# Optimization experiments

Measured on AMD Instinct MI355X. Metric: run time of the kernel, lower is better.

The kernel has to match this reference:

```python
import jax, jax.numpy as jnp
import numpy as np

E, D, DFF = 8, 1024, 4096

def setup_inputs() -> dict:
    key = jax.random.key(0)
    ks = jax.random.split(key, 10)
    s = 0.02
    return {
        "x":  jax.random.normal(ks[0], (4, 2048, D), dtype=jnp.float32),
        "Wr": jax.random.normal(ks[1], (D, E), dtype=jnp.float32) * s,
        "br": jnp.zeros((E,), dtype=jnp.float32),
        "W1": jax.random.normal(ks[2], (E, D, DFF), dtype=jnp.float32) * s,
        "b1": jnp.zeros((E, DFF), dtype=jnp.float32),
        "W2": jax.random.normal(ks[3], (E, D, DFF), dtype=jnp.float32) * s,
        "b2": jnp.zeros((E, DFF), dtype=jnp.float32),
        "W3": jax.random.normal(ks[4], (E, DFF, D), dtype=jnp.float32) * s,
        "b3": jnp.zeros((E, D), dtype=jnp.float32),
    }

def reference(x, Wr, br, W1, b1, W2, b2, W3, b3):
    b, s, d = x.shape
    xt = x.reshape(b * s, d)                       # [T, D]
    logits = xt @ Wr + br                          # [T, E]
    pr, idx = jax.lax.top_k(logits, 2)             # [T, 2]
    w = jax.nn.softmax(pr, axis=-1)                # softmax over the 2 selected experts
    # combine weight per (token, expert): sum of routing weights where expert selected
    onehot = jax.nn.one_hot(idx, W1.shape[0], dtype=x.dtype)  # [T, 2, E]
    cw = jnp.einsum('tk,tke->te', w, onehot)       # [T, E]
    y = jnp.zeros_like(xt)
    for e in range(W1.shape[0]):                   # small fixed expert loop
        h = jax.nn.silu(xt @ W1[e] + b1[e]) * (xt @ W2[e] + b2[e])  # SwiGLU [T, DFF]
        y = y + (h @ W3[e] + b3[e]) * cw[:, e:e + 1]
    return y.reshape(b, s, d)
```

## Files before the change

kernel.cpp:

```cpp
#include <hip/hip_runtime.h>

#define T_TOK 8192
#define DIM   1024
#define DFF_  4096
#define NE    8
#define MAXT  144

typedef float  f32x4 __attribute__((ext_vector_type(4)));
typedef __bf16 b16x8 __attribute__((ext_vector_type(8)));
typedef unsigned short u16x4 __attribute__((ext_vector_type(4)));

__device__ __forceinline__ unsigned short f2bf(float f) {
  union { float f; unsigned int u; } v; v.f = f;
  unsigned int r = v.u + 0x7fffu + ((v.u >> 16) & 1u);
  return (unsigned short)(r >> 16);
}

__device__ __forceinline__ void gload_lds16(const void* g, void* l) {
  __builtin_amdgcn_global_load_lds((const __attribute__((address_space(1))) void*)g,
                                   (__attribute__((address_space(3))) void*)l,
                                   16, 0, 0);
}

#define DRAIN_VMCNT() asm volatile("s_waitcnt vmcnt(0)" ::: "memory")

__global__ __launch_bounds__(256) void transpose_cvt(const float* __restrict__ src,
                                                     unsigned short* __restrict__ dst,
                                                     int R, int C) {
  __shared__ float tile[64][68];
  size_t mat = (size_t)blockIdx.z * R * C;
  int c0 = blockIdx.x * 64, r0 = blockIdx.y * 64;
  int t = threadIdx.x;
  int rcol = (t & 15) * 4, rrow = t >> 4;
  const float* s = src + mat + (size_t)r0 * C + c0;
#pragma unroll
  for (int i = 0; i < 4; i++) {
    int r = rrow + i * 16;
    f32x4 v = *(const f32x4*)(s + (size_t)r * C + rcol);
    *(f32x4*)(&tile[r][rcol]) = v;
  }
  __syncthreads();
  unsigned short* d = dst + mat + (size_t)c0 * R + r0;
  int wrow4 = (t & 15) * 4, wcol = t >> 4;
#pragma unroll
  for (int i = 0; i < 4; i++) {
    int cc = wcol + i * 16;
    u16x4 o;
    o[0] = f2bf(tile[wrow4 + 0][cc]);
    o[1] = f2bf(tile[wrow4 + 1][cc]);
    o[2] = f2bf(tile[wrow4 + 2][cc]);
    o[3] = f2bf(tile[wrow4 + 3][cc]);
    *(u16x4*)(&d[(size_t)cc * R + wrow4]) = o;
  }
}

__global__ __launch_bounds__(256) void router_k(const float* __restrict__ x,
                                                const float* __restrict__ Wr,
                                                const float* __restrict__ br,
                                                unsigned short* __restrict__ Xbf,
                                                int* __restrict__ top2e,
                                                float* __restrict__ top2w,
                                                int* __restrict__ counts) {
  __shared__ int lcnt[NE];
  if (threadIdx.x < NE) lcnt[threadIdx.x] = 0;
  __syncthreads();
  int wid = threadIdx.x >> 6, lane = threadIdx.x & 63;
  int t = blockIdx.x * 4 + wid;
  const float* xr = x + (size_t)t * DIM;
  unsigned short* xb = Xbf + (size_t)t * DIM;
  float s[NE];
#pragma unroll
  for (int e = 0; e < NE; e++) s[e] = 0.f;
  for (int i = 0; i < DIM / 64; i++) {
    int dd = i * 64 + lane;
    float xv = xr[dd];
    xb[dd] = f2bf(xv);
    const float* w = Wr + (size_t)dd * NE;
#pragma unroll
    for (int e = 0; e < NE; e++) s[e] += xv * w[e];
  }
#pragma unroll
  for (int m = 32; m >= 1; m >>= 1) {
#pragma unroll
    for (int e = 0; e < NE; e++) s[e] += __shfl_xor(s[e], m, 64);
  }
  if (lane == 0) {
#pragma unroll
    for (int e = 0; e < NE; e++) s[e] += br[e];
    int e0 = 0;
#pragma unroll
    for (int e = 1; e < NE; e++) if (s[e] > s[e0]) e0 = e;
    int e1 = (e0 == 0) ? 1 : 0;
#pragma unroll
    for (int e = 0; e < NE; e++) if (e != e0 && s[e] > s[e1]) e1 = e;
    float w0 = 1.f / (1.f + expf(s[e1] - s[e0]));
    top2e[2 * t] = e0; top2e[2 * t + 1] = e1;
    top2w[2 * t] = w0; top2w[2 * t + 1] = 1.f - w0;
    atomicAdd(&lcnt[e0], 1);
    atomicAdd(&lcnt[e1], 1);
  }
  __syncthreads();
  if (threadIdx.x < NE) atomicAdd(&counts[threadIdx.x], lcnt[threadIdx.x]);
}

__global__ void scan_build(int* __restrict__ ctrl) {
  if (threadIdx.x != 0 || blockIdx.x != 0) return;
  int* counts = ctrl;
  int* offsets = ctrl + 8;
  int* cursors = ctrl + 16;
  int* nt256 = ctrl + 24;
  int* tE256 = ctrl + 32;
  int* tM256 = ctrl + 32 + MAXT;
  int o = 0;
  for (int e = 0; e < NE; e++) { offsets[e] = o; cursors[e] = o; o += counts[e]; }
  int a = 0;
  for (int e = 0; e < NE; e++)
    for (int m0 = 0; m0 < counts[e]; m0 += 256) { tE256[a] = e; tM256[a] = m0; a++; }
  nt256[0] = a;
}

__global__ __launch_bounds__(256) void scatter_k(const int* __restrict__ top2e,
                                                 const float* __restrict__ top2w,
                                                 int* __restrict__ cursors,
                                                 int* __restrict__ list_tok,
                                                 float* __restrict__ list_w) {
  __shared__ int lcnt[NE];
  __shared__ int lbase[NE];
  int tid = threadIdx.x;
  if (tid < NE) lcnt[tid] = 0;
  __syncthreads();
  int t = blockIdx.x * 256 + tid;
  int e0 = top2e[2 * t], e1 = top2e[2 * t + 1];
  int r0 = atomicAdd(&lcnt[e0], 1);
  int r1 = atomicAdd(&lcnt[e1], 1);
  __syncthreads();
  if (tid < NE) lbase[tid] = atomicAdd(&cursors[tid], lcnt[tid]);
  __syncthreads();
  int p0 = lbase[e0] + r0, p1 = lbase[e1] + r1;
  list_tok[p0] = t; list_w[p0] = top2w[2 * t];
  list_tok[p1] = t; list_w[p1] = top2w[2 * t + 1];
}

__global__ __launch_bounds__(1024, 4) void gemm1_k(const unsigned short* __restrict__ Xbf,
                                                   const unsigned short* __restrict__ W1T,
                                                   const unsigned short* __restrict__ W2T,
                                                   const float* __restrict__ b1,
                                                   const float* __restrict__ b2,
                                                   unsigned short* __restrict__ H,
                                                   const int* __restrict__ list_tok,
                                                   const int* __restrict__ ctrl) {
  const int* counts = ctrl; const int* offsets = ctrl + 8;
  const int* ntile = ctrl + 24;
  const int* tileE = ctrl + 32; const int* tileM = ctrl + 32 + MAXT;
  int bt = blockIdx.y;
  if (bt >= ntile[0]) return;
  int e = tileE[bt], m0 = tileM[bt];
  int Me = counts[e], off = offsets[e];
  int n0 = blockIdx.x * 128;

  __shared__ unsigned short lds[2][32768];

  int tid = threadIdx.x, lane = tid & 63, wid = tid >> 6;
  int wr = wid >> 2, wc = wid & 3;

  const unsigned short* gsrc[4];
  unsigned ldsoff[4];
  {
    int lr = lane >> 3;
    int sc = ((lane & 7) ^ (lane >> 3)) * 8;
#pragma unroll
    for (int j = 0; j < 4; j++) {
      int c = wid * 4 + j;
      ldsoff[j] = c * 512;
      if (c < 32) {
        int r = c * 8 + lr;
        int tok = (m0 + r < Me) ? list_tok[off + m0 + r] : list_tok[off];
        gsrc[j] = Xbf + (size_t)tok * DIM + sc;
      } else if (c < 48) {
        int n = n0 + (c - 32) * 8 + lr;
        gsrc[j] = W1T + ((size_t)e * DFF_ + n) * DIM + sc;
      } else {
        int n = n0 + (c - 48) * 8 + lr;
        gsrc[j] = W2T + ((size_t)e * DFF_ + n) * DIM + sc;
      }
    }
  }

  unsigned aoff[2][4], boff[2][2];
  {
    int colg = lane >> 4;
#pragma unroll
    for (int kk = 0; kk < 2; kk++) {
#pragma unroll
      for (int m = 0; m < 4; m++) {
        int row = wr * 64 + m * 16 + (lane & 15);
        aoff[kk][m] = row * 64 + (((kk * 4 + colg) ^ (row & 7)) * 8);
      }
#pragma unroll
      for (int n = 0; n < 2; n++) {
        int row = wc * 32 + n * 16 + (lane & 15);
        boff[kk][n] = 16384 + row * 64 + (((kk * 4 + colg) ^ (row & 7)) * 8);
      }
    }
  }

  f32x4 acc1[4][2], acc2[4][2];
#pragma unroll
  for (int i = 0; i < 4; i++)
#pragma unroll
    for (int j = 0; j < 2; j++) {
      acc1[i][j] = f32x4{0.f, 0.f, 0.f, 0.f};
      acc2[i][j] = f32x4{0.f, 0.f, 0.f, 0.f};
    }

  auto compute = [&](const unsigned short* base) {
#pragma unroll
    for (int kk = 0; kk < 2; kk++) {
      b16x8 aF[4], bF1[2], bF2[2];
#pragma unroll
      for (int m = 0; m < 4; m++) aF[m] = *(const b16x8*)(base + aoff[kk][m]);
#pragma unroll
      for (int n = 0; n < 2; n++) {
        bF1[n] = *(const b16x8*)(base + boff[kk][n]);
        bF2[n] = *(const b16x8*)(base + boff[kk][n] + 8192);
      }
#pragma unroll
      for (int m = 0; m < 4; m++)
#pragma unroll
        for (int n = 0; n < 2; n++) {
          acc1[m][n] = __builtin_amdgcn_mfma_f32_16x16x32_bf16(aF[m], bF1[n], acc1[m][n], 0, 0, 0);
          acc2[m][n] = __builtin_amdgcn_mfma_f32_16x16x32_bf16(aF[m], bF2[n], acc2[m][n], 0, 0, 0);
        }
    }
  };

#pragma unroll
  for (int j = 0; j < 4; j++) gload_lds16(gsrc[j], (void*)(&lds[0][ldsoff[j]]));
  DRAIN_VMCNT();
  __syncthreads();

  int cur = 0;
  const int NK = DIM / 64;
  for (int kt = 0; kt < NK; kt++) {
    if (kt + 1 < NK) {
#pragma unroll
      for (int j = 0; j < 4; j++)
        gload_lds16(gsrc[j] + (kt + 1) * 64, (void*)(&lds[cur ^ 1][ldsoff[j]]));
    }
    compute(&lds[cur][0]);
    DRAIN_VMCNT();
    __syncthreads();
    cur ^= 1;
  }

#pragma unroll
  for (int n = 0; n < 2; n++) {
    int col = n0 + wc * 32 + n * 16 + (lane & 15);
    float bb1 = b1[e * DFF_ + col], bb2 = b2[e * DFF_ + col];
#pragma unroll
    for (int m = 0; m < 4; m++) {
      int rbase = wr * 64 + m * 16 + (lane >> 4) * 4;
#pragma unroll
      for (int r = 0; r < 4; r++) {
        int rr = rbase + r;
        if (m0 + rr < Me) {
          float c1 = acc1[m][n][r] + bb1;
          float c2 = acc2[m][n][r] + bb2;
          float h = c1 * c2 / (1.f + __expf(-c1));
          H[(size_t)(off + m0 + rr) * DFF_ + col] = f2bf(h);
        }
      }
    }
  }
}

__global__ __launch_bounds__(1024, 4) void gemm2_k(const unsigned short* __restrict__ H,
                                                   const unsigned short* __restrict__ W3T,
                                                   const float* __restrict__ b3,
                                                   const int* __restrict__ list_tok,
                                                   const float* __restrict__ list_w,
                                                   float* __restrict__ y,
                                                   const int* __restrict__ ctrl) {
  const int* counts = ctrl; const int* offsets = ctrl + 8;
  const int* ntile = ctrl + 24;
  const int* tileE = ctrl + 32; const int* tileM = ctrl + 32 + MAXT;
  int bt = blockIdx.y;
  if (bt >= ntile[0]) return;
  int e = tileE[bt], m0 = tileM[bt];
  int Me = counts[e], off = offsets[e];
  int n0 = blockIdx.x * 256;

  __shared__ unsigned short lds[2][32768];

  int tid = threadIdx.x, lane = tid & 63, wid = tid >> 6;
  int wr = wid >> 2, wc = wid & 3;

  const unsigned short* gsrc[4];
  unsigned ldsoff[4];
  {
    int lr = lane >> 3;
    int sc = ((lane & 7) ^ (lane >> 3)) * 8;
#pragma unroll
    for (int j = 0; j < 4; j++) {
      int c = wid * 4 + j;
      ldsoff[j] = c * 512;
      if (c < 32) {
        int r = c * 8 + lr;
        int pos = (m0 + r < Me) ? (off + m0 + r) : off;
        gsrc[j] = H + (size_t)pos * DFF_ + sc;
      } else {
        int n = n0 + (c - 32) * 8 + lr;
        gsrc[j] = W3T + ((size_t)e * DIM + n) * DFF_ + sc;
      }
    }
  }

  unsigned aoff[2][4], boff[2][4];
  {
    int colg = lane >> 4;
#pragma unroll
    for (int kk = 0; kk < 2; kk++) {
#pragma unroll
      for (int m = 0; m < 4; m++) {
        int row = wr * 64 + m * 16 + (lane & 15);
        aoff[kk][m] = row * 64 + (((kk * 4 + colg) ^ (row & 7)) * 8);
      }
#pragma unroll
      for (int n = 0; n < 4; n++) {
        int row = wc * 64 + n * 16 + (lane & 15);
        boff[kk][n] = 16384 + row * 64 + (((kk * 4 + colg) ^ (row & 7)) * 8);
      }
    }
  }

  f32x4 acc[4][4];
#pragma unroll
  for (int i = 0; i < 4; i++)
#pragma unroll
    for (int j = 0; j < 4; j++) acc[i][j] = f32x4{0.f, 0.f, 0.f, 0.f};

  auto compute = [&](const unsigned short* base) {
#pragma unroll
    for (int kk = 0; kk < 2; kk++) {
      b16x8 aF[4], bF[4];
#pragma unroll
      for (int m = 0; m < 4; m++) aF[m] = *(const b16x8*)(base + aoff[kk][m]);
#pragma unroll
      for (int n = 0; n < 4; n++) bF[n] = *(const b16x8*)(base + boff[kk][n]);
#pragma unroll
      for (int m = 0; m < 4; m++)
#pragma unroll
        for (int n = 0; n < 4; n++)
          acc[m][n] = __builtin_amdgcn_mfma_f32_16x16x32_bf16(aF[m], bF[n], acc[m][n], 0, 0, 0);
    }
  };

#pragma unroll
  for (int j = 0; j < 4; j++) gload_lds16(gsrc[j], (void*)(&lds[0][ldsoff[j]]));
  DRAIN_VMCNT();
  __syncthreads();

  int cur = 0;
  const int NK = DFF_ / 64;
  for (int kt = 0; kt < NK; kt++) {
    if (kt + 1 < NK) {
#pragma unroll
      for (int j = 0; j < 4; j++)
        gload_lds16(gsrc[j] + (kt + 1) * 64, (void*)(&lds[cur ^ 1][ldsoff[j]]));
    }
    compute(&lds[cur][0]);
    DRAIN_VMCNT();
    __syncthreads();
    cur ^= 1;
  }

#pragma unroll
  for (int n = 0; n < 4; n++) {
    int col = n0 + wc * 64 + n * 16 + (lane & 15);
    float bb3 = b3[e * DIM + col];
#pragma unroll
    for (int m = 0; m < 4; m++) {
      int rbase = wr * 64 + m * 16 + (lane >> 4) * 4;
#pragma unroll
      for (int r = 0; r < 4; r++) {
        int rr = rbase + r;
        if (m0 + rr < Me) {
          int pos = off + m0 + rr;
          float v = list_w[pos] * (acc[m][n][r] + bb3);
          atomicAdd(&y[(size_t)list_tok[pos] * DIM + col], v);
        }
      }
    }
  }
}

extern "C" void kernel_launch(void* const* d_in, const int* in_sizes, int n_in,
                              void* d_out, int out_size, void* d_ws, size_t ws_size,
                              hipStream_t stream) {
  (void)in_sizes; (void)n_in; (void)ws_size;
  const float* x  = (const float*)d_in[0];
  const float* Wr = (const float*)d_in[1];
  const float* br = (const float*)d_in[2];
  const float* W1 = (const float*)d_in[3];
  const float* b1 = (const float*)d_in[4];
  const float* W2 = (const float*)d_in[5];
  const float* b2 = (const float*)d_in[6];
  const float* W3 = (const float*)d_in[7];
  const float* b3 = (const float*)d_in[8];
  float* y = (float*)d_out;
  char* ws = (char*)d_ws;

  const size_t matB = (size_t)NE * DFF_ * DIM * 2;
  size_t oW1T = 0;
  size_t oW2T = oW1T + matB;
  size_t oXbf = oW2T + matB;
  size_t oH   = oXbf + (size_t)T_TOK * DIM * 2;
  size_t oT2e = oH + (size_t)2 * T_TOK * DFF_ * 2;
  size_t oT2w = oT2e + (size_t)2 * T_TOK * 4;
  size_t oLtk = oT2w + (size_t)2 * T_TOK * 4;
  size_t oLw  = oLtk + (size_t)2 * T_TOK * 4;
  size_t oCtl = oLw + (size_t)2 * T_TOK * 4;

  unsigned short* W1T = (unsigned short*)(ws + oW1T);
  unsigned short* W2T = (unsigned short*)(ws + oW2T);
  unsigned short* W3T = (unsigned short*)(ws + oW1T);
  unsigned short* Xbf = (unsigned short*)(ws + oXbf);
  unsigned short* Hb  = (unsigned short*)(ws + oH);
  int*   top2e = (int*)(ws + oT2e);
  float* top2w = (float*)(ws + oT2w);
  int*   ltok  = (int*)(ws + oLtk);
  float* lw    = (float*)(ws + oLw);
  int*   ctrl  = (int*)(ws + oCtl);

  hipMemsetAsync(y, 0, (size_t)out_size * 4, stream);
  hipMemsetAsync(ctrl, 0, (32 + 2 * MAXT) * 4, stream);

  transpose_cvt<<<dim3(DFF_ / 64, DIM / 64, NE), 256, 0, stream>>>(W1, W1T, DIM, DFF_);
  transpose_cvt<<<dim3(DFF_ / 64, DIM / 64, NE), 256, 0, stream>>>(W2, W2T, DIM, DFF_);
  router_k<<<dim3(T_TOK / 4), 256, 0, stream>>>(x, Wr, br, Xbf, top2e, top2w, ctrl);
  scan_build<<<dim3(1), 64, 0, stream>>>(ctrl);
  scatter_k<<<dim3(T_TOK / 256), 256, 0, stream>>>(top2e, top2w, ctrl + 16, ltok, lw);
  gemm1_k<<<dim3(DFF_ / 128, 71), 1024, 0, stream>>>(Xbf, W1T, W2T, b1, b2, Hb, ltok, ctrl);
  transpose_cvt<<<dim3(DIM / 64, DFF_ / 64, NE), 256, 0, stream>>>(W3, W3T, DFF_, DIM);
  gemm2_k<<<dim3(DIM / 256, 71), 1024, 0, stream>>>(Hb, W3T, b3, ltok, lw, y, ctrl);
}
```

Before: 706.7 us.

## Split-K gemm2, merge W1/W2 transposes, widen transpose and router accesses

gemm2 now splits the DFF reduction into two halves along grid z and accumulates both into y with atomics. Only the first half adds the bias, and the grid grows from 284 to 568 blocks to fill more CUs. The W1 and W2 transpose-convert launches are merged into one kernel. The transpose now uses an XOR-swizzled LDS tile with 8-wide bf16 stores, and the router loads x as float4 and writes four bf16 values at once. The cost is twice as many atomicAdds into y, and the order of float accumulation now varies between runs.

```diff
diff --git a/kernel.cpp b/kernel.cpp
--- a/kernel.cpp
+++ b/kernel.cpp
@@ -9,6 +9,7 @@
 typedef float  f32x4 __attribute__((ext_vector_type(4)));
 typedef __bf16 b16x8 __attribute__((ext_vector_type(8)));
 typedef unsigned short u16x4 __attribute__((ext_vector_type(4)));
+typedef unsigned short u16x8 __attribute__((ext_vector_type(8)));
 
 __device__ __forceinline__ unsigned short f2bf(float f) {
   union { float f; unsigned int u; } v; v.f = f;
@@ -24,34 +25,54 @@
 
 #define DRAIN_VMCNT() asm volatile("s_waitcnt vmcnt(0)" ::: "memory")
 
+__device__ __forceinline__ void tcvt_body(const float* __restrict__ src,
+                                          unsigned short* __restrict__ dst,
+                                          int R, int C, int bx, int by) {
+  __shared__ float tile[64 * 64];
+  int c0 = bx * 64, r0 = by * 64;
+  int t = threadIdx.x;
+  const float* s = src + (size_t)r0 * C + c0;
+  int rrow = t >> 4, c4r = t & 15;
+#pragma unroll
+  for (int i = 0; i < 4; i++) {
+    int r = rrow + i * 16;
+    f32x4 v = *(const f32x4*)(s + (size_t)r * C + c4r * 4);
+    int c4s = c4r ^ (r >> 3);
+    *(f32x4*)(&tile[r * 64 + c4s * 4]) = v;
+  }
+  __syncthreads();
+  unsigned short* d = dst + (size_t)c0 * R + r0;
+  int wr8 = (t & 7) * 8, wcol = t >> 3;
+#pragma unroll
+  for (int i = 0; i < 2; i++) {
+    int cc = wcol + i * 32;
+    u16x8 o;
+#pragma unroll
+    for (int j = 0; j < 8; j++) {
+      int r = wr8 + j;
+      int c4 = (cc >> 2) ^ (r >> 3);
+      o[j] = f2bf(tile[r * 64 + c4 * 4 + (cc & 3)]);
+    }
+    *(u16x8*)(&d[(size_t)cc * R + wr8]) = o;
+  }
+}
+
 __global__ __launch_bounds__(256) void transpose_cvt(const float* __restrict__ src,
                                                      unsigned short* __restrict__ dst,
                                                      int R, int C) {
-  __shared__ float tile[64][68];
   size_t mat = (size_t)blockIdx.z * R * C;
-  int c0 = blockIdx.x * 64, r0 = blockIdx.y * 64;
-  int t = threadIdx.x;
-  int rcol = (t & 15) * 4, rrow = t >> 4;
-  const float* s = src + mat + (size_t)r0 * C + c0;
-#pragma unroll
-  for (int i = 0; i < 4; i++) {
-    int r = rrow + i * 16;
-    f32x4 v = *(const f32x4*)(s + (size_t)r * C + rcol);
-    *(f32x4*)(&tile[r][rcol]) = v;
-  }
-  __syncthreads();
-  unsigned short* d = dst + mat + (size_t)c0 * R + r0;
-  int wrow4 = (t & 15) * 4, wcol = t >> 4;
-#pragma unroll
-  for (int i = 0; i < 4; i++) {
-    int cc = wcol + i * 16;
-    u16x4 o;
-    o[0] = f2bf(tile[wrow4 + 0][cc]);
-    o[1] = f2bf(tile[wrow4 + 1][cc]);
-    o[2] = f2bf(tile[wrow4 + 2][cc]);
-    o[3] = f2bf(tile[wrow4 + 3][cc]);
-    *(u16x4*)(&d[(size_t)cc * R + wrow4]) = o;
-  }
+  tcvt_body(src + mat, dst + mat, R, C, blockIdx.x, blockIdx.y);
+}
+
+__global__ __launch_bounds__(256) void transpose_cvt12(const float* __restrict__ W1,
+                                                       const float* __restrict__ W2,
+                                                       unsigned short* __restrict__ W1T,
+                                                       unsigned short* __restrict__ W2T) {
+  int z = blockIdx.z;
+  size_t mat = (size_t)(z & 7) * DIM * DFF_;
+  const float* src = (z < 8 ? W1 : W2) + mat;
+  unsigned short* dst = (z < 8 ? W1T : W2T) + mat;
+  tcvt_body(src, dst, DIM, DFF_, blockIdx.x, blockIdx.y);
 }
 
 __global__ __launch_bounds__(256) void router_k(const float* __restrict__ x,
@@ -71,13 +92,19 @@
   float s[NE];
 #pragma unroll
   for (int e = 0; e < NE; e++) s[e] = 0.f;
-  for (int i = 0; i < DIM / 64; i++) {
-    int dd = i * 64 + lane;
-    float xv = xr[dd];
-    xb[dd] = f2bf(xv);
-    const float* w = Wr + (size_t)dd * NE;
-#pragma unroll
-    for (int e = 0; e < NE; e++) s[e] += xv * w[e];
+  for (int i = 0; i < DIM / 256; i++) {
+    int dd = i * 256 + lane * 4;
+    f32x4 xv = *(const f32x4*)(xr + dd);
+    u16x4 xb4;
+#pragma unroll
+    for (int j = 0; j < 4; j++) xb4[j] = f2bf(xv[j]);
+    *(u16x4*)(&xb[dd]) = xb4;
+#pragma unroll
+    for (int j = 0; j < 4; j++) {
+      const float* w = Wr + (size_t)(dd + j) * NE;
+#pragma unroll
+      for (int e = 0; e < NE; e++) s[e] += xv[j] * w[e];
+    }
   }
 #pragma unroll
   for (int m = 32; m >= 1; m >>= 1) {
@@ -289,6 +316,7 @@
   int e = tileE[bt], m0 = tileM[bt];
   int Me = counts[e], off = offsets[e];
   int n0 = blockIdx.x * 256;
+  int koff = blockIdx.z * (DFF_ / 2);
 
   __shared__ unsigned short lds[2][32768];
 
@@ -307,10 +335,10 @@
       if (c < 32) {
         int r = c * 8 + lr;
         int pos = (m0 + r < Me) ? (off + m0 + r) : off;
-        gsrc[j] = H + (size_t)pos * DFF_ + sc;
+        gsrc[j] = H + (size_t)pos * DFF_ + koff + sc;
       } else {
         int n = n0 + (c - 32) * 8 + lr;
-        gsrc[j] = W3T + ((size_t)e * DIM + n) * DFF_ + sc;
+        gsrc[j] = W3T + ((size_t)e * DIM + n) * DFF_ + koff + sc;
       }
     }
   }
@@ -361,7 +389,7 @@
   __syncthreads();
 
   int cur = 0;
-  const int NK = DFF_ / 64;
+  const int NK = (DFF_ / 2) / 64;
   for (int kt = 0; kt < NK; kt++) {
     if (kt + 1 < NK) {
 #pragma unroll
@@ -374,10 +402,11 @@
     cur ^= 1;
   }
 
+  bool addb = (blockIdx.z == 0);
 #pragma unroll
   for (int n = 0; n < 4; n++) {
     int col = n0 + wc * 64 + n * 16 + (lane & 15);
-    float bb3 = b3[e * DIM + col];
+    float bb3 = addb ? b3[e * DIM + col] : 0.f;
 #pragma unroll
     for (int m = 0; m < 4; m++) {
       int rbase = wr * 64 + m * 16 + (lane >> 4) * 4;
@@ -435,12 +464,11 @@
   hipMemsetAsync(y, 0, (size_t)out_size * 4, stream);
   hipMemsetAsync(ctrl, 0, (32 + 2 * MAXT) * 4, stream);
 
-  transpose_cvt<<<dim3(DFF_ / 64, DIM / 64, NE), 256, 0, stream>>>(W1, W1T, DIM, DFF_);
-  transpose_cvt<<<dim3(DFF_ / 64, DIM / 64, NE), 256, 0, stream>>>(W2, W2T, DIM, DFF_);
+  transpose_cvt12<<<dim3(DFF_ / 64, DIM / 64, 2 * NE), 256, 0, stream>>>(W1, W2, W1T, W2T);
   router_k<<<dim3(T_TOK / 4), 256, 0, stream>>>(x, Wr, br, Xbf, top2e, top2w, ctrl);
   scan_build<<<dim3(1), 64, 0, stream>>>(ctrl);
   scatter_k<<<dim3(T_TOK / 256), 256, 0, stream>>>(top2e, top2w, ctrl + 16, ltok, lw);
   gemm1_k<<<dim3(DFF_ / 128, 71), 1024, 0, stream>>>(Xbf, W1T, W2T, b1, b2, Hb, ltok, ctrl);
   transpose_cvt<<<dim3(DIM / 64, DFF_ / 64, NE), 256, 0, stream>>>(W3, W3T, DFF_, DIM);
-  gemm2_k<<<dim3(DIM / 256, 71), 1024, 0, stream>>>(Hb, W3T, b3, ltok, lw, y, ctrl);
-}
+  gemm2_k<<<dim3(DIM / 256, 71, 2), 1024, 0, stream>>>(Hb, W3T, b3, ltok, lw, y, ctrl);
+}
```

Result: slower. 731.4 us (+3.5%).
